# Optimization experiments

Measured on AMD Instinct MI355X. Metric: run time of the kernel, lower is better.

The kernel has to match this reference:

```python
import jax, jax.numpy as jnp
import numpy as np

B, NS, F_IN, H, DEG = 128, 200, 200, 128, 64
N = B * NS
E = B * NS * DEG


def leaky_relu(v):
    return jnp.where(v > 0, v, 0.01 * v)


def gcn_conv(x, W, b, src, dst, w_pos):
    # PyG GCNConv with add_self_loops=True (self-loop weight 1) and
    # symmetric deg^{-1/2} normalization; aggregation flows src -> dst.
    n = x.shape[0]
    deg = jax.ops.segment_sum(w_pos, dst, num_segments=n) + 1.0  # +1 from self-loop
    dinv = jnp.where(deg > 0, deg ** -0.5, 0.0)
    norm = dinv[src] * w_pos * dinv[dst]          # [E]
    xw = x @ W                                     # [N,H]
    msg = norm[:, None] * xw[src]                  # [E,H]
    out = jax.ops.segment_sum(msg, dst, num_segments=n)
    out = out + (dinv * dinv)[:, None] * xw        # self-loop: norm = deg^{-1}
    return out + b


def setup_inputs() -> dict:
    key = jax.random.key(0)
    ks = jax.random.split(key, 14)
    # edges: each node gets DEG incoming edges from random nodes in SAME graph
    src_local = jax.random.randint(ks[0], (B, NS * DEG), 0, NS)
    dst_local = jnp.tile(jnp.repeat(jnp.arange(NS), DEG)[None, :], (B, 1))
    offsets = (jnp.arange(B) * NS)[:, None]
    src = (src_local + offsets).reshape(-1).astype(jnp.int32)
    dst = (dst_local + offsets).reshape(-1).astype(jnp.int32)
    edge_index = jnp.stack([src, dst])             # [2,E]
    edge_weight = jax.random.normal(ks[1], (E,), dtype=jnp.float32)  # mixed sign
    x = jax.random.normal(ks[2], (N, F_IN), dtype=jnp.float32)
    s = 0.05
    p = {
        'W0': jax.random.normal(ks[3], (F_IN, H)) * s, 'b0': jnp.zeros((H,)),
        'W1': jax.random.normal(ks[4], (H, H)) * s,    'b1': jnp.zeros((H,)),
        'W2': jax.random.normal(ks[5], (H, H)) * s,    'b2': jnp.zeros((H,)),
        'lincomb_W': jax.random.normal(ks[6], (NS * H, H)) * 0.01,
        'lincomb_b': jnp.zeros((H,)),
        'fc1_W': jax.random.normal(ks[7], (H, H // 2)) * s, 'fc1_b': jnp.zeros((H // 2,)),
        'fc2_W': jax.random.normal(ks[8], (H // 2, H // 4)) * s, 'fc2_b': jnp.zeros((H // 4,)),
        'fc3_W': jax.random.normal(ks[9], (H // 4, 1)) * s, 'fc3_b': jnp.zeros((1,)),
    }
    return {'x': x, 'edge_index': edge_index, 'edge_weight': edge_weight, **p}


def reference(x, edge_index, edge_weight,
              W0, b0, W1, b1, W2, b2,
              lincomb_W, lincomb_b,
              fc1_W, fc1_b, fc2_W, fc2_b, fc3_W, fc3_b):
    src, dst = edge_index[0], edge_index[1]
    # convert_edge_positive: dropping non-positive edges == zeroing their weight
    w_pos = jnp.where(edge_weight > 0, edge_weight, 0.0)
    h = gcn_conv(x, W0, b0, src, dst, w_pos)
    h = leaky_relu(h)
    h = gcn_conv(h, W1, b1, src, dst, w_pos)
    h = leaky_relu(h)
    h = gcn_conv(h, W2, b2, src, dst, w_pos)  # no activation on last layer
    # per-graph flatten + lincomb
    g = h.reshape(B, NS * H) @ lincomb_W + lincomb_b   # [B,H]
    g = leaky_relu(g @ fc1_W + fc1_b)
    g = leaky_relu(g @ fc2_W + fc2_b)
    out = g @ fc3_W + fc3_b                            # [B,1]
    return out
```

## Files before the change

### kernel.cpp

```cpp
#include <hip/hip_runtime.h>

#define B_GRAPHS 128
#define NSN      200
#define F_INPUT  200
#define HDIM     128
#define DEG      64
#define N_NODES  (B_GRAPHS * NSN)
#define E_EDGES  (N_NODES * DEG)

__global__ __launch_bounds__(256) void k_dinv(const float* __restrict__ ew,
                                              float* __restrict__ dinv) {
  const int node = blockIdx.x * 4 + (threadIdx.x >> 6);
  const int lane = threadIdx.x & 63;
  float w = ew[(size_t)node * DEG + lane];
  w = w > 0.f ? w : 0.f;
  #pragma unroll
  for (int off = 32; off > 0; off >>= 1) w += __shfl_down(w, off);
  if (lane == 0) dinv[node] = rsqrtf(w + 1.0f);
}

__global__ __launch_bounds__(256) void k_prep(const int* __restrict__ src,
                                              const float* __restrict__ ew,
                                              const float* __restrict__ dinv,
                                              int* __restrict__ csrc,
                                              float* __restrict__ cnrm,
                                              int* __restrict__ cntp) {
  const int node = blockIdx.x * 4 + (threadIdx.x >> 6);
  const int lane = threadIdx.x & 63;
  const int g = node / NSN;
  const size_t e = (size_t)node * DEG + lane;
  const float w = ew[e];
  const int s = src[e];
  const bool act = w > 0.f;
  float nv = act ? dinv[s] * w * dinv[node] : 0.f;
  const unsigned long long m = __ballot(act);
  const unsigned long long below = (lane == 63) ? ~0ull >> 1
                                                : ((1ull << lane) - 1ull);
  const int cnt = __popcll(m);
  const size_t base = (size_t)node * DEG;
  if (act) {
    const int pos = __popcll(m & below);
    csrc[base + pos] = s - g * NSN;
    cnrm[base + pos] = nv;
  } else {
    const int rank = __popcll(~m & below);
    csrc[base + cnt + rank] = 0;
    cnrm[base + cnt + rank] = 0.f;
  }
  if (lane == 0) cntp[node] = (cnt + 3) & ~3;
}

template <int F>
__global__ __launch_bounds__(256) void k_gemm(const float* __restrict__ X,
                                              const float* __restrict__ W,
                                              float* __restrict__ out) {
  __shared__ float Xs[64][8];
  __shared__ float Ws[8][128];
  const int t  = threadIdx.x;
  const int tx = t & 31;
  const int ty = t >> 5;
  const size_t row0 = (size_t)blockIdx.x * 64;
  float acc[8][4] = {};
  for (int k0 = 0; k0 < F; k0 += 8) {
    {
      const int i = t * 2;
      const int r = i >> 3, kk = i & 7;
      const float2 v = *reinterpret_cast<const float2*>(X + (row0 + r) * F + (k0 + kk));
      Xs[r][kk] = v.x; Xs[r][kk + 1] = v.y;
    }
    {
      const int j = t * 4;
      const int kk = j >> 7, col = j & 127;
      const float4 v = *reinterpret_cast<const float4*>(W + (size_t)(k0 + kk) * HDIM + col);
      *reinterpret_cast<float4*>(&Ws[kk][col]) = v;
    }
    __syncthreads();
    float xr[8][8];
    #pragma unroll
    for (int ii = 0; ii < 8; ++ii) {
      const float4 a = *reinterpret_cast<const float4*>(&Xs[ty * 8 + ii][0]);
      const float4 b = *reinterpret_cast<const float4*>(&Xs[ty * 8 + ii][4]);
      xr[ii][0] = a.x; xr[ii][1] = a.y; xr[ii][2] = a.z; xr[ii][3] = a.w;
      xr[ii][4] = b.x; xr[ii][5] = b.y; xr[ii][6] = b.z; xr[ii][7] = b.w;
    }
    #pragma unroll
    for (int kk = 0; kk < 8; ++kk) {
      const float4 wq = *reinterpret_cast<const float4*>(&Ws[kk][tx * 4]);
      const float wv[4] = {wq.x, wq.y, wq.z, wq.w};
      #pragma unroll
      for (int ii = 0; ii < 8; ++ii)
        #pragma unroll
        for (int jj = 0; jj < 4; ++jj)
          acc[ii][jj] = fmaf(xr[ii][kk], wv[jj], acc[ii][jj]);
    }
    __syncthreads();
  }
  #pragma unroll
  for (int ii = 0; ii < 8; ++ii) {
    const float4 v = {acc[ii][0], acc[ii][1], acc[ii][2], acc[ii][3]};
    *reinterpret_cast<float4*>(out + (row0 + ty * 8 + ii) * HDIM + tx * 4) = v;
  }
}

__global__ __launch_bounds__(512) void k_agg(const float* __restrict__ xw,
                                             const int* __restrict__ csrc,
                                             const float* __restrict__ cnrm,
                                             const int* __restrict__ cntp,
                                             const float* __restrict__ dinv,
                                             const float* __restrict__ bias,
                                             float* __restrict__ out,
                                             const int leaky) {
  __shared__ float xs[NSN * HDIM];
  const int g    = blockIdx.x >> 1;
  const int half = blockIdx.x & 1;
  const int t    = threadIdx.x;
  const int w    = t >> 6;
  const int lane = t & 63;

  {
    const float4* s4 = reinterpret_cast<const float4*>(xw + (size_t)g * NSN * HDIM);
    float4* d4 = reinterpret_cast<float4*>(xs);
    for (int i = t; i < NSN * HDIM / 4; i += 512) d4[i] = s4[i];
  }
  __syncthreads();

  const float2 bv = *reinterpret_cast<const float2*>(bias + lane * 2);
  const float2* xs2 = reinterpret_cast<const float2*>(xs);

  for (int nloc = half * 100 + w; nloc < half * 100 + 100; nloc += 8) {
    const int ng = g * NSN + nloc;
    const size_t base = (size_t)ng * DEG;
    const int   s_k = csrc[base + lane];
    const float n_k = cnrm[base + lane];
    const int  kmax = cntp[ng];
    float ax = 0.f, ay = 0.f;
    for (int k = 0; k < kmax; k += 4) {
      #pragma unroll
      for (int j = 0; j < 4; ++j) {
        const int   s  = __builtin_amdgcn_readlane(s_k, k + j);
        const float nv = __uint_as_float(
            __builtin_amdgcn_readlane(__float_as_uint(n_k), k + j));
        const float2 v = xs2[s * (HDIM / 2) + lane];
        ax = fmaf(nv, v.x, ax);
        ay = fmaf(nv, v.y, ay);
      }
    }
    const float di = dinv[ng];
    const float sc = di * di;
    const float2 xv = xs2[nloc * (HDIM / 2) + lane];
    ax = fmaf(sc, xv.x, ax) + bv.x;
    ay = fmaf(sc, xv.y, ay) + bv.y;
    if (leaky) {
      ax = ax > 0.f ? ax : 0.01f * ax;
      ay = ay > 0.f ? ay : 0.01f * ay;
    }
    *reinterpret_cast<float2*>(out + (size_t)ng * HDIM + lane * 2) = make_float2(ax, ay);
  }
}

__global__ __launch_bounds__(256) void k_lincomb(const float* __restrict__ h,
                                                 const float* __restrict__ Wl,
                                                 float* __restrict__ P) {
  const int i = blockIdx.x;
  __shared__ float As[128][8];
  __shared__ float Bs[8][128];
  const int t   = threadIdx.x;
  const int txx = t & 15;
  const int ty  = t >> 4;
  float acc[8][8] = {};
  for (int k0 = 0; k0 < HDIM; k0 += 8) {
    {
      const int idx = t * 4;
      const int r = idx >> 3, kk = idx & 7;
      const float4 v = *reinterpret_cast<const float4*>(
          h + ((size_t)r * NSN + i) * HDIM + k0 + kk);
      As[r][kk] = v.x; As[r][kk + 1] = v.y; As[r][kk + 2] = v.z; As[r][kk + 3] = v.w;
    }
    {
      const int idx = t * 4;
      const int kk = idx >> 7, col = idx & 127;
      const float4 v = *reinterpret_cast<const float4*>(
          Wl + ((size_t)i * HDIM + k0 + kk) * HDIM + col);
      *reinterpret_cast<float4*>(&Bs[kk][col]) = v;
    }
    __syncthreads();
    #pragma unroll
    for (int kk = 0; kk < 8; ++kk) {
      float av[8], bv[8];
      #pragma unroll
      for (int ii = 0; ii < 8; ++ii) av[ii] = As[ty * 8 + ii][kk];
      #pragma unroll
      for (int jj = 0; jj < 8; ++jj) bv[jj] = Bs[kk][txx + jj * 16];
      #pragma unroll
      for (int ii = 0; ii < 8; ++ii)
        #pragma unroll
        for (int jj = 0; jj < 8; ++jj)
          acc[ii][jj] = fmaf(av[ii], bv[jj], acc[ii][jj]);
    }
    __syncthreads();
  }
  #pragma unroll
  for (int ii = 0; ii < 8; ++ii)
    #pragma unroll
    for (int jj = 0; jj < 8; ++jj)
      P[((size_t)i * B_GRAPHS + ty * 8 + ii) * HDIM + txx + jj * 16] = acc[ii][jj];
}

__global__ __launch_bounds__(256) void k_reduce(const float* __restrict__ P,
                                                const float* __restrict__ bl,
                                                float* __restrict__ g) {
  const int idx = blockIdx.x * 256 + threadIdx.x;
  float s0 = 0.f, s1 = 0.f, s2 = 0.f, s3 = 0.f;
  #pragma unroll 4
  for (int i = 0; i < NSN; i += 4) {
    s0 += P[(size_t)(i + 0) * (B_GRAPHS * HDIM) + idx];
    s1 += P[(size_t)(i + 1) * (B_GRAPHS * HDIM) + idx];
    s2 += P[(size_t)(i + 2) * (B_GRAPHS * HDIM) + idx];
    s3 += P[(size_t)(i + 3) * (B_GRAPHS * HDIM) + idx];
  }
  g[idx] = (s0 + s1) + (s2 + s3) + bl[idx & 127];
}

__global__ __launch_bounds__(64) void k_fc(const float* __restrict__ g,
                                           const float* __restrict__ f1W,
                                           const float* __restrict__ f1b,
                                           const float* __restrict__ f2W,
                                           const float* __restrict__ f2b,
                                           const float* __restrict__ f3W,
                                           const float* __restrict__ f3b,
                                           float* __restrict__ out) {
  const int b = blockIdx.x, t = threadIdx.x;
  __shared__ float gb[128];
  __shared__ float a1[64];
  __shared__ float a2[32];
  gb[t]      = g[(size_t)b * HDIM + t];
  gb[t + 64] = g[(size_t)b * HDIM + t + 64];
  __syncthreads();
  float acc = f1b[t];
  #pragma unroll 8
  for (int c = 0; c < 128; ++c) acc = fmaf(gb[c], f1W[c * 64 + t], acc);
  a1[t] = acc > 0.f ? acc : 0.01f * acc;
  __syncthreads();
  if (t < 32) {
    float a = f2b[t];
    #pragma unroll 8
    for (int c = 0; c < 64; ++c) a = fmaf(a1[c], f2W[c * 32 + t], a);
    a2[t] = a > 0.f ? a : 0.01f * a;
  }
  __syncthreads();
  if (t == 0) {
    float a = f3b[0];
    #pragma unroll
    for (int c = 0; c < 32; ++c) a = fmaf(a2[c], f3W[c], a);
    out[b] = a;
  }
}

extern "C" void kernel_launch(void* const* d_in, const int* in_sizes, int n_in,
                              void* d_out, int out_size, void* d_ws, size_t ws_size,
                              hipStream_t stream) {
  const float* x   = (const float*)d_in[0];
  const int*   ei  = (const int*)  d_in[1];
  const float* ew  = (const float*)d_in[2];
  const float* W0  = (const float*)d_in[3];
  const float* b0  = (const float*)d_in[4];
  const float* W1  = (const float*)d_in[5];
  const float* b1  = (const float*)d_in[6];
  const float* W2  = (const float*)d_in[7];
  const float* b2  = (const float*)d_in[8];
  const float* Wl  = (const float*)d_in[9];
  const float* bl  = (const float*)d_in[10];
  const float* f1W = (const float*)d_in[11];
  const float* f1b = (const float*)d_in[12];
  const float* f2W = (const float*)d_in[13];
  const float* f2b = (const float*)d_in[14];
  const float* f3W = (const float*)d_in[15];
  const float* f3b = (const float*)d_in[16];
  float* out = (float*)d_out;

  const int* src = ei;

  float* dinv = (float*)d_ws;
  int*   csrc = (int*)(dinv + 32768);
  float* cnrm = (float*)(csrc + E_EDGES);
  int*   cntp = (int*)(cnrm + E_EDGES);
  float* xw   = (float*)(cntp + 32768);
  float* hA   = xw + (size_t)N_NODES * HDIM;
  float* P    = xw;
  float* g    = hA + (size_t)N_NODES * HDIM;

  k_dinv<<<N_NODES / 4, 256, 0, stream>>>(ew, dinv);
  k_prep<<<N_NODES / 4, 256, 0, stream>>>(src, ew, dinv, csrc, cnrm, cntp);

  k_gemm<F_INPUT><<<N_NODES / 64, 256, 0, stream>>>(x, W0, xw);
  k_agg<<<B_GRAPHS * 2, 512, 0, stream>>>(xw, csrc, cnrm, cntp, dinv, b0, hA, 1);
  k_gemm<HDIM><<<N_NODES / 64, 256, 0, stream>>>(hA, W1, xw);
  k_agg<<<B_GRAPHS * 2, 512, 0, stream>>>(xw, csrc, cnrm, cntp, dinv, b1, hA, 1);
  k_gemm<HDIM><<<N_NODES / 64, 256, 0, stream>>>(hA, W2, xw);
  k_agg<<<B_GRAPHS * 2, 512, 0, stream>>>(xw, csrc, cnrm, cntp, dinv, b2, hA, 0);

  k_lincomb<<<NSN, 256, 0, stream>>>(hA, Wl, P);
  k_reduce<<<(B_GRAPHS * HDIM) / 256, 256, 0, stream>>>(P, bl, g);
  k_fc<<<B_GRAPHS, 64, 0, stream>>>(g, f1W, f1b, f2W, f2b, f3W, f3b, out);
}
```

Before: 323.6 us.

## Unify GEMMs into 128x128-tile kernel and fuse reduce with FC head

Replaces the 64-row GEMM with a general 128x128-tile, K=16 GEMM that uses a transposed shared-memory A tile and an 8x8 per-thread microtile. The same kernel now serves the three per-layer GEMMs and the per-node lincomb batched GEMM through block strides. The separate partial-sum reduce and FC kernels are merged into one kernel, removing a launch and the intermediate g buffer. The aim is more register reuse and fewer launches. The cost is half as many blocks for the node GEMMs, which may lower occupancy.

```diff
diff --git a/kernel.cpp b/kernel.cpp
--- a/kernel.cpp
+++ b/kernel.cpp
@@ -51,54 +51,92 @@
 }
 
 template <int F>
-__global__ __launch_bounds__(256) void k_gemm(const float* __restrict__ X,
-                                              const float* __restrict__ W,
-                                              float* __restrict__ out) {
-  __shared__ float Xs[64][8];
-  __shared__ float Ws[8][128];
+__global__ __launch_bounds__(256) void k_gemm2(const float* __restrict__ A,
+                                               const long ablk, const long astride,
+                                               const float* __restrict__ W,
+                                               const long wblk,
+                                               float* __restrict__ out) {
+  __shared__ float XsT[16][132];
+  __shared__ float Ws[16][128];
   const int t  = threadIdx.x;
-  const int tx = t & 31;
-  const int ty = t >> 5;
-  const size_t row0 = (size_t)blockIdx.x * 64;
-  float acc[8][4] = {};
-  for (int k0 = 0; k0 < F; k0 += 8) {
-    {
-      const int i = t * 2;
-      const int r = i >> 3, kk = i & 7;
-      const float2 v = *reinterpret_cast<const float2*>(X + (row0 + r) * F + (k0 + kk));
-      Xs[r][kk] = v.x; Xs[r][kk + 1] = v.y;
-    }
-    {
-      const int j = t * 4;
-      const int kk = j >> 7, col = j & 127;
-      const float4 v = *reinterpret_cast<const float4*>(W + (size_t)(k0 + kk) * HDIM + col);
-      *reinterpret_cast<float4*>(&Ws[kk][col]) = v;
-    }
-    __syncthreads();
-    float xr[8][8];
-    #pragma unroll
-    for (int ii = 0; ii < 8; ++ii) {
-      const float4 a = *reinterpret_cast<const float4*>(&Xs[ty * 8 + ii][0]);
-      const float4 b = *reinterpret_cast<const float4*>(&Xs[ty * 8 + ii][4]);
-      xr[ii][0] = a.x; xr[ii][1] = a.y; xr[ii][2] = a.z; xr[ii][3] = a.w;
-      xr[ii][4] = b.x; xr[ii][5] = b.y; xr[ii][6] = b.z; xr[ii][7] = b.w;
-    }
-    #pragma unroll
-    for (int kk = 0; kk < 8; ++kk) {
-      const float4 wq = *reinterpret_cast<const float4*>(&Ws[kk][tx * 4]);
-      const float wv[4] = {wq.x, wq.y, wq.z, wq.w};
+  const int tx = t & 15;
+  const int ty = t >> 4;
+  const float* Ab = A + (size_t)blockIdx.x * ablk;
+  const float* Wb = W + (size_t)blockIdx.x * wblk;
+  float* ob = out + (size_t)blockIdx.x * (128 * 128);
+
+  float acc[8][8] = {};
+
+  constexpr int FC = F / 16;
+  for (int c = 0; c < FC; ++c) {
+    const int k0 = c * 16;
+    #pragma unroll
+    for (int q = 0; q < 2; ++q) {
+      const int idx = t * 2 + q;
+      const int r = idx >> 2, ks = (idx & 3) * 4;
+      const float4 v = *reinterpret_cast<const float4*>(Ab + (size_t)r * astride + k0 + ks);
+      XsT[ks + 0][r] = v.x; XsT[ks + 1][r] = v.y;
+      XsT[ks + 2][r] = v.z; XsT[ks + 3][r] = v.w;
+    }
+    #pragma unroll
+    for (int q = 0; q < 2; ++q) {
+      const int idx = t * 2 + q;
+      const int kk = idx >> 5, col4 = (idx & 31) * 4;
+      const float4 v = *reinterpret_cast<const float4*>(Wb + (size_t)(k0 + kk) * 128 + col4);
+      *reinterpret_cast<float4*>(&Ws[kk][col4]) = v;
+    }
+    __syncthreads();
+    #pragma unroll
+    for (int kk = 0; kk < 16; ++kk) {
+      float a8[8], w8[8];
+      *reinterpret_cast<float4*>(&a8[0]) = *reinterpret_cast<const float4*>(&XsT[kk][ty * 8]);
+      *reinterpret_cast<float4*>(&a8[4]) = *reinterpret_cast<const float4*>(&XsT[kk][ty * 8 + 4]);
+      *reinterpret_cast<float4*>(&w8[0]) = *reinterpret_cast<const float4*>(&Ws[kk][tx * 8]);
+      *reinterpret_cast<float4*>(&w8[4]) = *reinterpret_cast<const float4*>(&Ws[kk][tx * 8 + 4]);
       #pragma unroll
       for (int ii = 0; ii < 8; ++ii)
         #pragma unroll
-        for (int jj = 0; jj < 4; ++jj)
-          acc[ii][jj] = fmaf(xr[ii][kk], wv[jj], acc[ii][jj]);
-    }
-    __syncthreads();
-  }
+        for (int jj = 0; jj < 8; ++jj)
+          acc[ii][jj] = fmaf(a8[ii], w8[jj], acc[ii][jj]);
+    }
+    __syncthreads();
+  }
+
+  if constexpr (F % 16 == 8) {
+    const int k0 = FC * 16;
+    {
+      const int r = t >> 1, ks = (t & 1) * 4;
+      const float4 v = *reinterpret_cast<const float4*>(Ab + (size_t)r * astride + k0 + ks);
+      XsT[ks + 0][r] = v.x; XsT[ks + 1][r] = v.y;
+      XsT[ks + 2][r] = v.z; XsT[ks + 3][r] = v.w;
+    }
+    {
+      const int kk = t >> 5, col4 = (t & 31) * 4;
+      const float4 v = *reinterpret_cast<const float4*>(Wb + (size_t)(k0 + kk) * 128 + col4);
+      *reinterpret_cast<float4*>(&Ws[kk][col4]) = v;
+    }
+    __syncthreads();
+    #pragma unroll
+    for (int kk = 0; kk < 8; ++kk) {
+      float a8[8], w8[8];
+      *reinterpret_cast<float4*>(&a8[0]) = *reinterpret_cast<const float4*>(&XsT[kk][ty * 8]);
+      *reinterpret_cast<float4*>(&a8[4]) = *reinterpret_cast<const float4*>(&XsT[kk][ty * 8 + 4]);
+      *reinterpret_cast<float4*>(&w8[0]) = *reinterpret_cast<const float4*>(&Ws[kk][tx * 8]);
+      *reinterpret_cast<float4*>(&w8[4]) = *reinterpret_cast<const float4*>(&Ws[kk][tx * 8 + 4]);
+      #pragma unroll
+      for (int ii = 0; ii < 8; ++ii)
+        #pragma unroll
+        for (int jj = 0; jj < 8; ++jj)
+          acc[ii][jj] = fmaf(a8[ii], w8[jj], acc[ii][jj]);
+    }
+    __syncthreads();
+  }
+
   #pragma unroll
   for (int ii = 0; ii < 8; ++ii) {
-    const float4 v = {acc[ii][0], acc[ii][1], acc[ii][2], acc[ii][3]};
-    *reinterpret_cast<float4*>(out + (row0 + ty * 8 + ii) * HDIM + tx * 4) = v;
+    float* o = ob + (size_t)(ty * 8 + ii) * 128 + tx * 8;
+    *reinterpret_cast<float4*>(o)     = make_float4(acc[ii][0], acc[ii][1], acc[ii][2], acc[ii][3]);
+    *reinterpret_cast<float4*>(o + 4) = make_float4(acc[ii][4], acc[ii][5], acc[ii][6], acc[ii][7]);
   }
 }
 
@@ -158,88 +196,36 @@
   }
 }
 
-__global__ __launch_bounds__(256) void k_lincomb(const float* __restrict__ h,
-                                                 const float* __restrict__ Wl,
-                                                 float* __restrict__ P) {
-  const int i = blockIdx.x;
-  __shared__ float As[128][8];
-  __shared__ float Bs[8][128];
-  const int t   = threadIdx.x;
-  const int txx = t & 15;
-  const int ty  = t >> 4;
-  float acc[8][8] = {};
-  for (int k0 = 0; k0 < HDIM; k0 += 8) {
-    {
-      const int idx = t * 4;
-      const int r = idx >> 3, kk = idx & 7;
-      const float4 v = *reinterpret_cast<const float4*>(
-          h + ((size_t)r * NSN + i) * HDIM + k0 + kk);
-      As[r][kk] = v.x; As[r][kk + 1] = v.y; As[r][kk + 2] = v.z; As[r][kk + 3] = v.w;
-    }
-    {
-      const int idx = t * 4;
-      const int kk = idx >> 7, col = idx & 127;
-      const float4 v = *reinterpret_cast<const float4*>(
-          Wl + ((size_t)i * HDIM + k0 + kk) * HDIM + col);
-      *reinterpret_cast<float4*>(&Bs[kk][col]) = v;
-    }
-    __syncthreads();
-    #pragma unroll
-    for (int kk = 0; kk < 8; ++kk) {
-      float av[8], bv[8];
-      #pragma unroll
-      for (int ii = 0; ii < 8; ++ii) av[ii] = As[ty * 8 + ii][kk];
-      #pragma unroll
-      for (int jj = 0; jj < 8; ++jj) bv[jj] = Bs[kk][txx + jj * 16];
-      #pragma unroll
-      for (int ii = 0; ii < 8; ++ii)
-        #pragma unroll
-        for (int jj = 0; jj < 8; ++jj)
-          acc[ii][jj] = fmaf(av[ii], bv[jj], acc[ii][jj]);
-    }
-    __syncthreads();
-  }
-  #pragma unroll
-  for (int ii = 0; ii < 8; ++ii)
-    #pragma unroll
-    for (int jj = 0; jj < 8; ++jj)
-      P[((size_t)i * B_GRAPHS + ty * 8 + ii) * HDIM + txx + jj * 16] = acc[ii][jj];
-}
-
-__global__ __launch_bounds__(256) void k_reduce(const float* __restrict__ P,
-                                                const float* __restrict__ bl,
-                                                float* __restrict__ g) {
-  const int idx = blockIdx.x * 256 + threadIdx.x;
-  float s0 = 0.f, s1 = 0.f, s2 = 0.f, s3 = 0.f;
-  #pragma unroll 4
-  for (int i = 0; i < NSN; i += 4) {
-    s0 += P[(size_t)(i + 0) * (B_GRAPHS * HDIM) + idx];
-    s1 += P[(size_t)(i + 1) * (B_GRAPHS * HDIM) + idx];
-    s2 += P[(size_t)(i + 2) * (B_GRAPHS * HDIM) + idx];
-    s3 += P[(size_t)(i + 3) * (B_GRAPHS * HDIM) + idx];
-  }
-  g[idx] = (s0 + s1) + (s2 + s3) + bl[idx & 127];
-}
-
-__global__ __launch_bounds__(64) void k_fc(const float* __restrict__ g,
-                                           const float* __restrict__ f1W,
-                                           const float* __restrict__ f1b,
-                                           const float* __restrict__ f2W,
-                                           const float* __restrict__ f2b,
-                                           const float* __restrict__ f3W,
-                                           const float* __restrict__ f3b,
-                                           float* __restrict__ out) {
+__global__ __launch_bounds__(128) void k_rfc(const float* __restrict__ P,
+                                             const float* __restrict__ bl,
+                                             const float* __restrict__ f1W,
+                                             const float* __restrict__ f1b,
+                                             const float* __restrict__ f2W,
+                                             const float* __restrict__ f2b,
+                                             const float* __restrict__ f3W,
+                                             const float* __restrict__ f3b,
+                                             float* __restrict__ out) {
   const int b = blockIdx.x, t = threadIdx.x;
   __shared__ float gb[128];
   __shared__ float a1[64];
   __shared__ float a2[32];
-  gb[t]      = g[(size_t)b * HDIM + t];
-  gb[t + 64] = g[(size_t)b * HDIM + t + 64];
-  __syncthreads();
-  float acc = f1b[t];
-  #pragma unroll 8
-  for (int c = 0; c < 128; ++c) acc = fmaf(gb[c], f1W[c * 64 + t], acc);
-  a1[t] = acc > 0.f ? acc : 0.01f * acc;
+  float s0 = 0.f, s1 = 0.f, s2 = 0.f, s3 = 0.f;
+  const float* p = P + (size_t)b * HDIM + t;
+  #pragma unroll 4
+  for (int i = 0; i < NSN; i += 4) {
+    s0 += p[(size_t)(i + 0) * (B_GRAPHS * HDIM)];
+    s1 += p[(size_t)(i + 1) * (B_GRAPHS * HDIM)];
+    s2 += p[(size_t)(i + 2) * (B_GRAPHS * HDIM)];
+    s3 += p[(size_t)(i + 3) * (B_GRAPHS * HDIM)];
+  }
+  gb[t] = (s0 + s1) + (s2 + s3) + bl[t];
+  __syncthreads();
+  if (t < 64) {
+    float acc = f1b[t];
+    #pragma unroll 8
+    for (int c = 0; c < 128; ++c) acc = fmaf(gb[c], f1W[c * 64 + t], acc);
+    a1[t] = acc > 0.f ? acc : 0.01f * acc;
+  }
   __syncthreads();
   if (t < 32) {
     float a = f2b[t];
@@ -287,19 +273,18 @@
   float* xw   = (float*)(cntp + 32768);
   float* hA   = xw + (size_t)N_NODES * HDIM;
   float* P    = xw;
-  float* g    = hA + (size_t)N_NODES * HDIM;
 
   k_dinv<<<N_NODES / 4, 256, 0, stream>>>(ew, dinv);
   k_prep<<<N_NODES / 4, 256, 0, stream>>>(src, ew, dinv, csrc, cnrm, cntp);
 
-  k_gemm<F_INPUT><<<N_NODES / 64, 256, 0, stream>>>(x, W0, xw);
+  k_gemm2<F_INPUT><<<N_NODES / 128, 256, 0, stream>>>(x, 128L * F_INPUT, F_INPUT, W0, 0, xw);
   k_agg<<<B_GRAPHS * 2, 512, 0, stream>>>(xw, csrc, cnrm, cntp, dinv, b0, hA, 1);
-  k_gemm<HDIM><<<N_NODES / 64, 256, 0, stream>>>(hA, W1, xw);
+  k_gemm2<HDIM><<<N_NODES / 128, 256, 0, stream>>>(hA, 128L * HDIM, HDIM, W1, 0, xw);
   k_agg<<<B_GRAPHS * 2, 512, 0, stream>>>(xw, csrc, cnrm, cntp, dinv, b1, hA, 1);
-  k_gemm<HDIM><<<N_NODES / 64, 256, 0, stream>>>(hA, W2, xw);
+  k_gemm2<HDIM><<<N_NODES / 128, 256, 0, stream>>>(hA, 128L * HDIM, HDIM, W2, 0, xw);
   k_agg<<<B_GRAPHS * 2, 512, 0, stream>>>(xw, csrc, cnrm, cntp, dinv, b2, hA, 0);
 
-  k_lincomb<<<NSN, 256, 0, stream>>>(hA, Wl, P);
-  k_reduce<<<(B_GRAPHS * HDIM) / 256, 256, 0, stream>>>(P, bl, g);
-  k_fc<<<B_GRAPHS, 64, 0, stream>>>(g, f1W, f1b, f2W, f2b, f3W, f3b, out);
-}
+  k_gemm2<HDIM><<<NSN, 256, 0, stream>>>(hA, (long)HDIM, (long)NSN * HDIM,
+                                         Wl, (long)HDIM * HDIM, P);
+  k_rfc<<<B_GRAPHS, 128, 0, stream>>>(P, bl, f1W, f1b, f2W, f2b, f3W, f3b, out);
+}
```

Result: no change. 322.2 us (-0.4%).
